# Kernel optimization log

Measured on AMD Instinct MI355X. Metric: run time of the kernel, lower is better.

Reference implementation:

```python
import jax, jax.numpy as jnp
import numpy as np

HDIM = 1024
CDIM = 256
TEMPER = 10.0
IGNORE_OUT = 0.0
EPS = 1e-6


def setup_inputs() -> dict:
    key = jax.random.key(0)
    ks = jax.random.split(key, 6)
    B, T, D = 2, 128, 384
    x = jax.random.normal(ks[0], (B, T, D), jnp.float32)
    y = jax.random.normal(ks[1], (B, T, D), jnp.float32)
    # xavier-normal style init for the two linear layers
    W_enc = jax.random.normal(ks[2], (D, HDIM), jnp.float32) * np.sqrt(2.0 / (D + HDIM))
    b_enc = jnp.zeros((HDIM,), jnp.float32)
    W_dec = jax.random.normal(ks[3], (HDIM, D), jnp.float32) * np.sqrt(2.0 / (D + HDIM))
    b_dec = jnp.zeros((D,), jnp.float32)
    return {"x": x, "y": y, "W_enc": W_enc, "b_enc": b_enc, "W_dec": W_dec, "b_dec": b_dec}


def reference(x, y, W_enc, b_enc, W_dec, b_dec):
    B, T, D = x.shape
    n_iter = HDIM // CDIM
    pad = D - 1
    # shift_idx[s, j] = s + j : window of width D at offset s, s in [0, 2D-2]
    shift_idx = jnp.arange(2 * D - 1)[:, None] + jnp.arange(D)[None, :]

    seq_mask = (y == IGNORE_OUT)                       # (B,T,D) bool
    denom_seq = jnp.sum(~seq_mask).astype(x.dtype)
    qn = jnp.linalg.norm(y, axis=-1)                   # (B,T)

    mask_prev = None
    x_dis, losses = [], []
    for _ in range(n_iter):
        # --- _pad_for_shift: (B,T,2D-1,D) shifted windows of x ---
        kp = jnp.pad(x, ((0, 0), (0, 0), (pad, pad)))  # (B,T,3D-2)
        kpt = kp[..., shift_idx]                       # (B,T,2D-1,D)
        # --- _score (cos) + argmax over shifts ---
        kn = jnp.linalg.norm(kpt, axis=-1)             # (B,T,2D-1)
        sim = jnp.einsum('btsd,btd->bts', kpt, y) / (qn[..., None] * kn + EPS)
        sim = jnp.where(jnp.isnan(sim), 0.0, sim)
        theta = jnp.argmax(sim, axis=-1)               # (B,T) int
        x_opt = jnp.take_along_axis(kpt, theta[..., None, None], axis=-2)[..., 0, :]  # (B,T,D)
        # --- attention: elementwise cos-scaled score, temp softmax, detached ---
        dn = (jnp.linalg.norm(x_opt, axis=-1, keepdims=True)
              * jnp.linalg.norm(y, axis=-1, keepdims=True) + EPS)
        attn = jax.nn.softmax((x_opt * y / dn) / TEMPER, axis=-1)
        attn = jnp.where(jnp.isnan(attn), 0.0, attn)
        attn = jax.lax.stop_gradient(attn)
        x_attn = x_opt * attn
        # --- _reverse_pad_for_shift: window at offset 2D-2-theta ---
        kp2 = jnp.pad(x_attn, ((0, 0), (0, 0), (pad, pad)))
        rev_idx = (2 * D - 2 - theta)[..., None] + jnp.arange(D)  # (B,T,D)
        x_ele = jnp.take_along_axis(kp2, rev_idx, axis=-1)         # (B,T,D)
        # --- self_net: encoder -> top-k sparsify -> decoder_self ---
        h = x_ele @ W_enc + b_enc                      # (B,T,HDIM)
        if mask_prev is not None:
            h = jnp.where(mask_prev > 0, 1e-10, h)
        _, idx_top = jax.lax.top_k(h, CDIM)            # (B,T,CDIM)
        flat = idx_top.reshape(B * T, CDIM)
        mask_cur = jnp.zeros((B * T, HDIM), x.dtype).at[
            jnp.arange(B * T)[:, None], flat].set(1.0).reshape(B, T, HDIM)
        if mask_prev is None:
            mask_prev = mask_cur
        else:
            mask_prev = mask_prev + mask_cur - mask_prev * mask_cur
        h = h * mask_cur
        out = h @ W_dec + b_dec                        # (B,T,D)
        x_dis.append(out)
        # --- SeqLoss (masked MSE, mean-reduced by count of valid elems) ---
        err = jnp.where(seq_mask, 0.0, (out - x) ** 2) / denom_seq
        losses.append(jnp.sum(err))
    return jnp.stack(x_dis), jnp.stack(losses)
```

## Files before the change

### kernel.cpp

```cpp
#include <hip/hip_runtime.h>
#include <math.h>

#define DD 384
#define HD 1024
#define CD 256
#define NS 765
#define NITER 4
#define NROWS 256
#define TEMPER_F 10.0f
#define EPSF 1e-6f
#define CUTF 1e-10f

typedef unsigned long long u64;
typedef unsigned int u32;

__device__ __forceinline__ u32 flipf(float f) {
    u32 u = __float_as_uint(f);
    return u ^ ((u32)((int)u >> 31) | 0x80000000u);
}
__device__ __forceinline__ float unflipf(u32 s) {
    u32 fl = ~s;
    u32 u = (fl & 0x80000000u) ? (fl ^ 0x80000000u) : ~fl;
    return __uint_as_float(u);
}
__device__ __forceinline__ u64 shflx64(u64 v, int m) {
    int lo = __shfl_xor((int)(u32)v, m, 64);
    int hi = __shfl_xor((int)(u32)(v >> 32), m, 64);
    return ((u64)(u32)hi << 32) | (u32)lo;
}
__device__ __forceinline__ u32 bf16r(float f) {
    u32 u = __float_as_uint(f);
    return (u + 0x7FFFu + ((u >> 16) & 1u)) >> 16;
}
__device__ __forceinline__ u32 pack2(float a, float b) {
    return bf16r(a) | (bf16r(b) << 16);
}
__device__ __forceinline__ float blo(u32 p) { return __uint_as_float(p << 16); }
__device__ __forceinline__ float bhi(u32 p) { return __uint_as_float(p & 0xFFFF0000u); }

__global__ __launch_bounds__(256) void convert_kernel(
    const float* __restrict__ We, const float* __restrict__ Wd,
    uint2* __restrict__ we16, uint2* __restrict__ wd16)
{
    const int t = blockIdx.x * 256 + threadIdx.x;
    for (int i = t; i < (DD * HD) / 4; i += 65536) {
        float4 v = ((const float4*)We)[i];
        we16[i] = make_uint2(pack2(v.x, v.y), pack2(v.z, v.w));
    }
    for (int i = t; i < (HD * DD) / 4; i += 65536) {
        float4 v = ((const float4*)Wd)[i];
        wd16[i] = make_uint2(pack2(v.x, v.y), pack2(v.z, v.w));
    }
}

__global__ __launch_bounds__(1024) void fused_kernel(
    const float* __restrict__ x, const float* __restrict__ y,
    const u32* __restrict__ wenc16, const float* __restrict__ benc,
    const u32* __restrict__ wdec16, const float* __restrict__ bdec,
    float* __restrict__ out_xdis, float* __restrict__ lossp,
    int* __restrict__ ycnt)
{
    const int row  = blockIdx.x;
    const int tid  = threadIdx.x;
    const int lane = tid & 63;
    const int wid  = tid >> 6;

    __shared__ __align__(16) float xpad[1152];
    __shared__ __align__(16) float yr[DD];
    __shared__ float xa[DD];
    __shared__ __align__(16) float xe_s[DD];
    __shared__ __align__(16) float part[4][HD];
    __shared__ __align__(16) u64   skey[HD];
    __shared__ __align__(16) uint2 dec2[HD];
    __shared__ float wred[16];
    __shared__ int   wredi[16];
    __shared__ float wredn[16];
    __shared__ float s_sc[4];
    __shared__ int   s_theta, s_fb;
    __shared__ float loss4[NITER];

    const float* xrow = x + row * DD;
    const float* yrow = y + row * DD;

    for (int i = tid; i < 1152; i += 1024)
        xpad[i] = (i >= DD - 1 && i < 2 * DD - 1) ? xrow[i - (DD - 1)] : 0.f;
    if (tid < DD) yr[tid] = yrow[tid];
    __syncthreads();

    if (tid < DD) {
        float p = yr[tid] * yr[tid];
        int   c = (yr[tid] != 0.f) ? 1 : 0;
        for (int o = 32; o; o >>= 1) {
            p += __shfl_xor(p, o, 64);
            c += __shfl_xor(c, o, 64);
        }
        if (lane == 0) { wred[wid] = p; wredi[wid] = c; }
    }
    __syncthreads();
    if (tid == 0) {
        float s = 0.f; int c = 0;
        for (int w = 0; w < 6; ++w) { s += wred[w]; c += wredi[w]; }
        s_sc[0] = sqrtf(s);
        ycnt[row] = c;
    }
    __syncthreads();
    const float qn = s_sc[0];

    float bv = -INFINITY; int bs = 0x7fffffff; float bn = 0.f;
    if (tid < 192) {
        const float4* xp4 = (const float4*)xpad;
        const float4* yp4 = (const float4*)yr;
        float4 A = xp4[tid];
        const float f0 = A.x * A.x, f1 = A.y * A.y, f2 = A.z * A.z;
        float d0 = 0.f, d1 = 0.f, d2 = 0.f, d3 = 0.f, n0 = 0.f;
#pragma unroll 4
        for (int jc = 0; jc < 96; ++jc) {
            float4 B = xp4[tid + jc + 1];
            float4 Y = yp4[jc];
            d0 += A.x * Y.x; d0 += A.y * Y.y; d0 += A.z * Y.z; d0 += A.w * Y.w;
            d1 += A.y * Y.x; d1 += A.z * Y.y; d1 += A.w * Y.z; d1 += B.x * Y.w;
            d2 += A.z * Y.x; d2 += A.w * Y.y; d2 += B.x * Y.z; d2 += B.y * Y.w;
            d3 += A.w * Y.x; d3 += B.x * Y.y; d3 += B.y * Y.z; d3 += B.z * Y.w;
            n0 += A.x * A.x; n0 += A.y * A.y; n0 += A.z * A.z; n0 += A.w * A.w;
            A = B;
        }
        const float n1 = n0 - f0 + A.x * A.x;
        const float n2 = n1 - f1 + A.y * A.y;
        const float n3 = n2 - f2 + A.z * A.z;
        const int s0 = 4 * tid;
        float sim0 = d0 / (qn * sqrtf(n0) + EPSF);
        float sim1 = d1 / (qn * sqrtf(n1) + EPSF);
        float sim2 = d2 / (qn * sqrtf(n2) + EPSF);
        float sim3 = d3 / (qn * sqrtf(n3) + EPSF);
        bv = sim0; bs = s0; bn = n0;
        if (s0 + 1 < NS && sim1 > bv) { bv = sim1; bs = s0 + 1; bn = n1; }
        if (s0 + 2 < NS && sim2 > bv) { bv = sim2; bs = s0 + 2; bn = n2; }
        if (s0 + 3 < NS && sim3 > bv) { bv = sim3; bs = s0 + 3; bn = n3; }
    }
    for (int o = 32; o; o >>= 1) {
        float v2 = __shfl_xor(bv, o, 64);
        int   i2 = __shfl_xor(bs, o, 64);
        float n2 = __shfl_xor(bn, o, 64);
        if (v2 > bv || (v2 == bv && i2 < bs)) { bv = v2; bs = i2; bn = n2; }
    }
    if (lane == 0) { wred[wid] = bv; wredi[wid] = bs; wredn[wid] = bn; }
    __syncthreads();
    if (tid == 0) {
        float v = wred[0]; int b = wredi[0]; float nn = wredn[0];
        for (int w = 1; w < 16; ++w)
            if (wred[w] > v || (wred[w] == v && wredi[w] < b)) {
                v = wred[w]; b = wredi[w]; nn = wredn[w];
            }
        s_theta = b;
        s_sc[1] = sqrtf(nn) * qn + EPSF;
    }
    __syncthreads();
    const int theta = s_theta;
    const float dn = s_sc[1];

    float xo = 0.f, z = 0.f;
    if (tid < DD) {
        xo = xpad[theta + tid];
        z = (xo * yr[tid] / dn) / TEMPER_F;
        float m = z;
        for (int o = 32; o; o >>= 1) { float w2 = __shfl_xor(m, o, 64); if (w2 > m) m = w2; }
        if (lane == 0) wred[wid] = m;
    }
    __syncthreads();
    if (tid == 0) {
        float m = wred[0];
        for (int w = 1; w < 6; ++w) if (wred[w] > m) m = wred[w];
        s_sc[2] = m;
    }
    __syncthreads();
    float ez = 0.f;
    if (tid < DD) {
        ez = expf(z - s_sc[2]);
        float p = ez;
        for (int o = 32; o; o >>= 1) p += __shfl_xor(p, o, 64);
        if (lane == 0) wred[wid] = p;
    }
    __syncthreads();
    if (tid == 0) {
        float s = 0.f;
        for (int w = 0; w < 6; ++w) s += wred[w];
        s_sc[3] = s;
    }
    __syncthreads();
    if (tid < DD) xa[tid] = xo * (ez / s_sc[3]);
    __syncthreads();
    if (tid < DD) {
        int sj = tid - (theta - (DD - 1));
        xe_s[tid] = (sj >= 0 && sj < DD) ? xa[sj] : 0.f;
    }
    __syncthreads();

    {
        const int ks = tid >> 8;
        const int c4 = tid & 255;
        const u32* wbase = wenc16 + (size_t)(ks * 96) * 512 + 2 * c4;
        const float* xb = xe_s + ks * 96;
        float4 acc = make_float4(0.f, 0.f, 0.f, 0.f);
#pragma unroll 8
        for (int j = 0; j < 96; ++j) {
            float xv = xb[j];
            uint2 wv = *(const uint2*)(wbase + (size_t)j * 512);
            acc.x += xv * blo(wv.x); acc.y += xv * bhi(wv.x);
            acc.z += xv * blo(wv.y); acc.w += xv * bhi(wv.y);
        }
        *(float4*)&part[ks][4 * c4] = acc;
    }
    if (tid == 0) s_fb = HD;
    if (tid < NITER) loss4[tid] = 0.f;
    __syncthreads();

    u64 e;
    {
        float hv = part[0][tid] + part[1][tid] + part[2][tid] + part[3][tid]
                 + benc[tid];
        e = ((u64)(~flipf(hv)) << 32) | (u32)tid;
    }

    for (int k = 2; k <= HD; k <<= 1) {
        const bool up = (tid & k) == 0;
        for (int j = k >> 1; j > 0; j >>= 1) {
            if (j <= 32) {
                u64 p = shflx64(e, j);
                const bool takeMin = ((tid & j) == 0) == up;
                e = takeMin ? (e < p ? e : p) : (e > p ? e : p);
            } else {
                __syncthreads();
                skey[tid] = e;
                __syncthreads();
                u64 p = skey[tid ^ j];
                const bool takeMin = ((tid & j) == 0) == up;
                e = takeMin ? (e < p ? e : p) : (e > p ? e : p);
            }
        }
    }

    {
        float v = unflipf((u32)(e >> 32));
        dec2[tid] = make_uint2(__float_as_uint(v), ((u32)e) * 192);
        int fbloc = (v > CUTF) ? HD : tid;
        for (int o = 32; o; o >>= 1) { int t2 = __shfl_xor(fbloc, o, 64); if (t2 < fbloc) fbloc = t2; }
        if (lane == 0) atomicMin(&s_fb, fbloc);
    }
    __syncthreads();
    const int fb = s_fb;

    {
        const int k = tid >> 8;
        const int g = tid & 255;
        const bool active = (g < 192);
        int n = 0;
        if (active) {
            n = (k == 0) ? CD : fb - k * CD;
            if (n < 0) n = 0; if (n > CD) n = CD;
        }
        float2 oacc = make_float2(0.f, 0.f);
        if (active) oacc = *(const float2*)&bdec[2 * g];
        const u32* wd = wdec16 + g;
        const int base = k * CD;
        int r = 0;
        for (; r + 8 <= n; r += 8) {
#pragma unroll
            for (int q = 0; q < 8; q += 2) {
                uint4 dv = *(const uint4*)&dec2[base + r + q];
                float v0 = __uint_as_float(dv.x);
                u32 w0 = wd[dv.y];
                float v1 = __uint_as_float(dv.z);
                u32 w1 = wd[dv.w];
                oacc.x += v0 * blo(w0); oacc.y += v0 * bhi(w0);
                oacc.x += v1 * blo(w1); oacc.y += v1 * bhi(w1);
            }
        }
        for (; r < n; ++r) {
            uint2 dv = dec2[base + r];
            float v0 = __uint_as_float(dv.x);
            u32 w0 = wd[dv.y];
            oacc.x += v0 * blo(w0); oacc.y += v0 * bhi(w0);
        }
        float l = 0.f;
        if (active) {
            *(float2*)&out_xdis[((size_t)k * NROWS + row) * DD + 2 * g] = oacc;
            float2 xv = *(const float2*)&xrow[2 * g];
            float2 yv = *(const float2*)&yr[2 * g];
            float ee;
            ee = oacc.x - xv.x; if (yv.x != 0.f) l += ee * ee;
            ee = oacc.y - xv.y; if (yv.y != 0.f) l += ee * ee;
        }
        for (int o = 32; o; o >>= 1) l += __shfl_xor(l, o, 64);
        if (lane == 0) atomicAdd(&loss4[k], l);
    }
    __syncthreads();
    if (tid < NITER) lossp[row * NITER + tid] = loss4[tid];
}

__global__ __launch_bounds__(256) void finalize2(
    const float* __restrict__ lossp, const int* __restrict__ ycnt,
    float* __restrict__ losses)
{
    const int tid = threadIdx.x, lane = tid & 63, w = tid >> 6;
    __shared__ int ctot[4];
    int c = ycnt[tid];
    for (int o = 32; o; o >>= 1) c += __shfl_xor(c, o, 64);
    if (lane == 0) ctot[w] = c;
    __syncthreads();
    const int total = ctot[0] + ctot[1] + ctot[2] + ctot[3];
    float s = lossp[lane * NITER + w] + lossp[(lane + 64) * NITER + w]
            + lossp[(lane + 128) * NITER + w] + lossp[(lane + 192) * NITER + w];
    for (int o = 32; o; o >>= 1) s += __shfl_xor(s, o, 64);
    if (lane == 0) losses[w] = s / (float)total;
}

extern "C" void kernel_launch(void* const* d_in, const int* in_sizes, int n_in,
                              void* d_out, int out_size, void* d_ws, size_t ws_size,
                              hipStream_t stream) {
    const float* x    = (const float*)d_in[0];
    const float* y    = (const float*)d_in[1];
    const float* Wenc = (const float*)d_in[2];
    const float* benc = (const float*)d_in[3];
    const float* Wdec = (const float*)d_in[4];
    const float* bdec = (const float*)d_in[5];

    float* out  = (float*)d_out;
    float* loss = out + (out_size - NITER);

    float* lossp  = (float*)d_ws;
    int*   ycnt   = (int*)(lossp + NROWS * NITER);
    u32*   wenc16 = (u32*)(ycnt + NROWS);
    u32*   wdec16 = wenc16 + (DD * HD) / 2;

    convert_kernel<<<256, 256, 0, stream>>>(Wenc, Wdec, (uint2*)wenc16, (uint2*)wdec16);
    fused_kernel<<<NROWS, 1024, 0, stream>>>(x, y, wenc16, benc, wdec16, bdec,
                                             out, lossp, ycnt);
    finalize2<<<1, 256, 0, stream>>>(lossp, ycnt, loss);
}
```

Measured before the change: 109.8 us.

## Use fp16 dot2 encoder, 32-bit bitonic keys, and ballot-based top-k compaction

The encoder weights are repacked as fp16 pairs interleaved along the input dimension, so the encoder GEMV uses packed fp16 dot2 instructions with half the loads. The bitonic sort now uses 32-bit keys without the index and double-buffers shared memory to drop one barrier per stage. Group boundaries are read from the sorted keys, and ballot/prefix-scan compaction builds the decoder list in place of the index-carrying sort. The softmax max-subtraction pass is removed, trading a reduction and barriers for overflow risk. fp16 activations lose precision, and equal keys now give non-deterministic tie handling.

```diff
diff --git a/kernel.cpp b/kernel.cpp
--- a/kernel.cpp
+++ b/kernel.cpp
@@ -1,4 +1,5 @@
 #include <hip/hip_runtime.h>
+#include <hip/hip_fp16.h>
 #include <math.h>
 
 #define DD 384
@@ -13,49 +14,55 @@
 
 typedef unsigned long long u64;
 typedef unsigned int u32;
+typedef _Float16 hh2 __attribute__((ext_vector_type(2)));
 
 __device__ __forceinline__ u32 flipf(float f) {
     u32 u = __float_as_uint(f);
     return u ^ ((u32)((int)u >> 31) | 0x80000000u);
 }
-__device__ __forceinline__ float unflipf(u32 s) {
-    u32 fl = ~s;
-    u32 u = (fl & 0x80000000u) ? (fl ^ 0x80000000u) : ~fl;
-    return __uint_as_float(u);
-}
-__device__ __forceinline__ u64 shflx64(u64 v, int m) {
-    int lo = __shfl_xor((int)(u32)v, m, 64);
-    int hi = __shfl_xor((int)(u32)(v >> 32), m, 64);
-    return ((u64)(u32)hi << 32) | (u32)lo;
-}
 __device__ __forceinline__ u32 bf16r(float f) {
     u32 u = __float_as_uint(f);
     return (u + 0x7FFFu + ((u >> 16) & 1u)) >> 16;
 }
-__device__ __forceinline__ u32 pack2(float a, float b) {
+__device__ __forceinline__ u32 pack2bf(float a, float b) {
     return bf16r(a) | (bf16r(b) << 16);
 }
 __device__ __forceinline__ float blo(u32 p) { return __uint_as_float(p << 16); }
 __device__ __forceinline__ float bhi(u32 p) { return __uint_as_float(p & 0xFFFF0000u); }
+__device__ __forceinline__ u32 packh2(float a, float b) {
+    __half2 p = __floats2half2_rn(a, b);
+    return __builtin_bit_cast(u32, p);
+}
+__device__ __forceinline__ float dot2(u32 a, u32 b, float c) {
+#if __has_builtin(__builtin_amdgcn_fdot2)
+    return __builtin_amdgcn_fdot2(__builtin_bit_cast(hh2, a),
+                                  __builtin_bit_cast(hh2, b), c, false);
+#else
+    __half2 ah = __builtin_bit_cast(__half2, a);
+    __half2 bh = __builtin_bit_cast(__half2, b);
+    return fmaf(__half2float(ah.y), __half2float(bh.y),
+           fmaf(__half2float(ah.x), __half2float(bh.x), c));
+#endif
+}
 
 __global__ __launch_bounds__(256) void convert_kernel(
     const float* __restrict__ We, const float* __restrict__ Wd,
-    uint2* __restrict__ we16, uint2* __restrict__ wd16)
+    u32* __restrict__ wencp, uint2* __restrict__ wd16)
 {
     const int t = blockIdx.x * 256 + threadIdx.x;
-    for (int i = t; i < (DD * HD) / 4; i += 65536) {
-        float4 v = ((const float4*)We)[i];
-        we16[i] = make_uint2(pack2(v.x, v.y), pack2(v.z, v.w));
+    for (int i = t; i < 192 * HD; i += 65536) {
+        int j2 = i >> 10, c = i & 1023;
+        wencp[i] = packh2(We[(2 * j2) * HD + c], We[(2 * j2 + 1) * HD + c]);
     }
     for (int i = t; i < (HD * DD) / 4; i += 65536) {
         float4 v = ((const float4*)Wd)[i];
-        wd16[i] = make_uint2(pack2(v.x, v.y), pack2(v.z, v.w));
+        wd16[i] = make_uint2(pack2bf(v.x, v.y), pack2bf(v.z, v.w));
     }
 }
 
 __global__ __launch_bounds__(1024) void fused_kernel(
     const float* __restrict__ x, const float* __restrict__ y,
-    const u32* __restrict__ wenc16, const float* __restrict__ benc,
+    const u32* __restrict__ wencp, const float* __restrict__ benc,
     const u32* __restrict__ wdec16, const float* __restrict__ bdec,
     float* __restrict__ out_xdis, float* __restrict__ lossp,
     int* __restrict__ ycnt)
@@ -69,14 +76,19 @@
     __shared__ __align__(16) float yr[DD];
     __shared__ float xa[DD];
     __shared__ __align__(16) float xe_s[DD];
+    __shared__ u32   xep[192];
     __shared__ __align__(16) float part[4][HD];
-    __shared__ __align__(16) u64   skey[HD];
+    __shared__ u32   sk0[HD], sk1[HD];
     __shared__ __align__(16) uint2 dec2[HD];
     __shared__ float wred[16];
     __shared__ int   wredi[16];
     __shared__ float wredn[16];
     __shared__ float s_sc[4];
-    __shared__ int   s_theta, s_fb;
+    __shared__ int   s_theta;
+    __shared__ u32   s_b1, s_b2, s_b3;
+    __shared__ int   wcls[128];
+    __shared__ int   sbase[128];
+    __shared__ int   cnt8[8];
     __shared__ float loss4[NITER];
 
     const float* xrow = x + row * DD;
@@ -158,24 +170,10 @@
     const int theta = s_theta;
     const float dn = s_sc[1];
 
-    float xo = 0.f, z = 0.f;
+    float xo = 0.f, ez = 0.f;
     if (tid < DD) {
         xo = xpad[theta + tid];
-        z = (xo * yr[tid] / dn) / TEMPER_F;
-        float m = z;
-        for (int o = 32; o; o >>= 1) { float w2 = __shfl_xor(m, o, 64); if (w2 > m) m = w2; }
-        if (lane == 0) wred[wid] = m;
-    }
-    __syncthreads();
-    if (tid == 0) {
-        float m = wred[0];
-        for (int w = 1; w < 6; ++w) if (wred[w] > m) m = wred[w];
-        s_sc[2] = m;
-    }
-    __syncthreads();
-    float ez = 0.f;
-    if (tid < DD) {
-        ez = expf(z - s_sc[2]);
+        ez = expf((xo * yr[tid] / dn) / TEMPER_F);
         float p = ez;
         for (int o = 32; o; o >>= 1) p += __shfl_xor(p, o, 64);
         if (lane == 0) wred[wid] = p;
@@ -194,70 +192,100 @@
         xe_s[tid] = (sj >= 0 && sj < DD) ? xa[sj] : 0.f;
     }
     __syncthreads();
+    if (tid < 192) xep[tid] = packh2(xe_s[2 * tid], xe_s[2 * tid + 1]);
+    __syncthreads();
 
     {
         const int ks = tid >> 8;
         const int c4 = tid & 255;
-        const u32* wbase = wenc16 + (size_t)(ks * 96) * 512 + 2 * c4;
-        const float* xb = xe_s + ks * 96;
+        const uint4* wq = (const uint4*)wencp + (size_t)(ks * 48) * 256 + c4;
+        const u32* xb = xep + ks * 48;
         float4 acc = make_float4(0.f, 0.f, 0.f, 0.f);
 #pragma unroll 8
-        for (int j = 0; j < 96; ++j) {
-            float xv = xb[j];
-            uint2 wv = *(const uint2*)(wbase + (size_t)j * 512);
-            acc.x += xv * blo(wv.x); acc.y += xv * bhi(wv.x);
-            acc.z += xv * blo(wv.y); acc.w += xv * bhi(wv.y);
+        for (int j2 = 0; j2 < 48; ++j2) {
+            u32 xv = xb[j2];
+            uint4 w = wq[(size_t)j2 * 256];
+            acc.x = dot2(xv, w.x, acc.x);
+            acc.y = dot2(xv, w.y, acc.y);
+            acc.z = dot2(xv, w.z, acc.z);
+            acc.w = dot2(xv, w.w, acc.w);
         }
         *(float4*)&part[ks][4 * c4] = acc;
     }
-    if (tid == 0) s_fb = HD;
+    if (tid < 8) cnt8[tid] = 0;
     if (tid < NITER) loss4[tid] = 0.f;
     __syncthreads();
 
-    u64 e;
+    float oh;
+    u32 okey, e;
     {
-        float hv = part[0][tid] + part[1][tid] + part[2][tid] + part[3][tid]
-                 + benc[tid];
-        e = ((u64)(~flipf(hv)) << 32) | (u32)tid;
-    }
-
+        oh = part[0][tid] + part[1][tid] + part[2][tid] + part[3][tid] + benc[tid];
+        okey = ~flipf(oh);
+        e = okey;
+    }
+
+    int par = 0;
     for (int k = 2; k <= HD; k <<= 1) {
         const bool up = (tid & k) == 0;
         for (int j = k >> 1; j > 0; j >>= 1) {
             if (j <= 32) {
-                u64 p = shflx64(e, j);
+                u32 p = __shfl_xor(e, j, 64);
                 const bool takeMin = ((tid & j) == 0) == up;
                 e = takeMin ? (e < p ? e : p) : (e > p ? e : p);
             } else {
+                u32* buf = par ? sk1 : sk0; par ^= 1;
+                buf[tid] = e;
                 __syncthreads();
-                skey[tid] = e;
-                __syncthreads();
-                u64 p = skey[tid ^ j];
+                u32 p = buf[tid ^ j];
                 const bool takeMin = ((tid & j) == 0) == up;
                 e = takeMin ? (e < p ? e : p) : (e > p ? e : p);
             }
         }
     }
+    if (tid == 255) s_b1 = e;
+    if (tid == 511) s_b2 = e;
+    if (tid == 767) s_b3 = e;
+    __syncthreads();
+    const u32 b1 = s_b1, b2 = s_b2, b3 = s_b3;
 
     {
-        float v = unflipf((u32)(e >> 32));
-        dec2[tid] = make_uint2(__float_as_uint(v), ((u32)e) * 192);
-        int fbloc = (v > CUTF) ? HD : tid;
-        for (int o = 32; o; o >>= 1) { int t2 = __shfl_xor(fbloc, o, 64); if (t2 < fbloc) fbloc = t2; }
-        if (lane == 0) atomicMin(&s_fb, fbloc);
-    }
-    __syncthreads();
-    const int fb = s_fb;
+        const int myk = (okey <= b1) ? 0 : (okey <= b2) ? 1 : (okey <= b3) ? 2 : 3;
+        const int cls = 2 * myk + ((oh > CUTF) ? 0 : 1);
+        int myprefix = 0;
+        const u64 ltmask = (1ull << lane) - 1;
+#pragma unroll
+        for (int c = 0; c < 8; ++c) {
+            u64 m = __ballot(cls == c);
+            if (cls == c) myprefix = __popcll(m & ltmask);
+            if (lane == 0) {
+                wcls[c * 16 + wid] = (int)__popcll(m);
+                atomicAdd(&cnt8[c], (int)__popcll(m));
+            }
+        }
+        __syncthreads();
+        if (tid < 128) {
+            int v = wcls[tid];
+            int inc = v;
+            for (int o = 1; o < 64; o <<= 1) {
+                int t2 = __shfl_up(inc, o, 64);
+                if (lane >= o) inc += t2;
+            }
+            sbase[tid] = inc - v;
+        }
+        __syncthreads();
+        if (tid >= 64 && tid < 128) sbase[tid] += sbase[63] + wcls[63];
+        __syncthreads();
+        const int slot = sbase[cls * 16 + wid] + myprefix;
+        dec2[slot] = make_uint2(__float_as_uint(oh), (u32)tid * 192u);
+    }
+    __syncthreads();
 
     {
         const int k = tid >> 8;
         const int g = tid & 255;
         const bool active = (g < 192);
         int n = 0;
-        if (active) {
-            n = (k == 0) ? CD : fb - k * CD;
-            if (n < 0) n = 0; if (n > CD) n = CD;
-        }
+        if (active) n = (k == 0) ? CD : cnt8[2 * k];
         float2 oacc = make_float2(0.f, 0.f);
         if (active) oacc = *(const float2*)&bdec[2 * g];
         const u32* wd = wdec16 + g;
@@ -329,11 +357,11 @@
 
     float* lossp  = (float*)d_ws;
     int*   ycnt   = (int*)(lossp + NROWS * NITER);
-    u32*   wenc16 = (u32*)(ycnt + NROWS);
-    u32*   wdec16 = wenc16 + (DD * HD) / 2;
-
-    convert_kernel<<<256, 256, 0, stream>>>(Wenc, Wdec, (uint2*)wenc16, (uint2*)wdec16);
-    fused_kernel<<<NROWS, 1024, 0, stream>>>(x, y, wenc16, benc, wdec16, bdec,
+    u32*   wencp  = (u32*)(ycnt + NROWS);
+    u32*   wdec16 = wencp + 192 * HD;
+
+    convert_kernel<<<256, 256, 0, stream>>>(Wenc, Wdec, wencp, (uint2*)wdec16);
+    fused_kernel<<<NROWS, 1024, 0, stream>>>(x, y, wencp, benc, wdec16, bdec,
                                              out, lossp, ycnt);
     finalize2<<<1, 256, 0, stream>>>(lossp, ycnt, loss);
 }
```

Result: faster. 106.2 us (-3.3%).
